# Performance work log

Hardware: AMD Instinct MI355X
Metric: run time of the kernel (lower is better)

The kernel has to match this reference:

```python
import jax, jax.numpy as jnp
import numpy as np

N, E, F_IN, HID, HEADS, OUT = 50000, 800000, 128, 64, 4, 40


def gat_layer(x, src, dst, n, W, a_src, a_dst, b, heads, ch):
    # PyG GATConv: h = x @ W per head; e_ij = LeakyReLU(a_src.h_j + a_dst.h_i)
    h = (x @ W).reshape(n, heads, ch)
    al_s = jnp.einsum('nhc,hc->nh', h, a_src)  # source-side logit term
    al_d = jnp.einsum('nhc,hc->nh', h, a_dst)  # target-side logit term
    e = jax.nn.leaky_relu(al_s[src] + al_d[dst], negative_slope=0.2)  # [E,H]
    m = jax.ops.segment_max(e, dst, num_segments=n)  # stable softmax per target node
    e = jnp.exp(e - m[dst])
    s = jax.ops.segment_sum(e, dst, num_segments=n)
    alpha = e / s[dst]  # [E,H]
    out = jax.ops.segment_sum(h[src] * alpha[:, :, None], dst, num_segments=n)  # [n,H,C]
    return out.reshape(n, heads * ch) + b


def gat_forward(x, src, dst, W0, as0, ad0, b0, W1, as1, ad1, b1, W2, as2, ad2, b2):
    n = x.shape[0]
    x = jax.nn.elu(gat_layer(x, src, dst, n, W0, as0, ad0, b0, HEADS, HID))
    x = jax.nn.elu(gat_layer(x, src, dst, n, W1, as1, ad1, b1, HEADS, HID))
    x = gat_layer(x, src, dst, n, W2, as2, ad2, b2, 1, OUT)
    return jax.nn.log_softmax(x, axis=1)


def setup_inputs() -> dict:
    key = jax.random.key(0)
    ks = jax.random.split(key, 16)
    x = jax.random.normal(ks[0], (N, F_IN), dtype=jnp.float32)
    edge_index = jax.random.randint(ks[1], (2, E), 0, N, dtype=jnp.int64)
    g = lambda k, sh: jax.random.normal(k, sh, dtype=jnp.float32) * (1.0 / np.sqrt(sh[0]))
    d_hid = HID * HEADS
    return {
        'x': x, 'edge_index': edge_index,
        'W0': g(ks[2], (F_IN, d_hid)), 'as0': g(ks[3], (HEADS, HID)), 'ad0': g(ks[4], (HEADS, HID)), 'b0': jnp.zeros((d_hid,), jnp.float32),
        'W1': g(ks[5], (d_hid, d_hid)), 'as1': g(ks[6], (HEADS, HID)), 'ad1': g(ks[7], (HEADS, HID)), 'b1': jnp.zeros((d_hid,), jnp.float32),
        'W2': g(ks[8], (d_hid, OUT)), 'as2': g(ks[9], (1, OUT)), 'ad2': g(ks[10], (1, OUT)), 'b2': jnp.zeros((OUT,), jnp.float32),
    }


def reference(x, edge_index, W0, as0, ad0, b0, W1, as1, ad1, b1, W2, as2, ad2, b2):
    n = x.shape[0]
    loops = jnp.arange(n, dtype=edge_index.dtype)  # PyG add_self_loops=True
    src = jnp.concatenate([edge_index[0], loops])
    dst = jnp.concatenate([edge_index[1], loops])
    return gat_forward(x, src, dst, W0, as0, ad0, b0, W1, as1, ad1, b1, W2, as2, ad2, b2)
```

## Files before the change

kernel.cpp:

```cpp
#include <hip/hip_runtime.h>
#include <hip/hip_fp16.h>
#include <math.h>

#define NODES 50000
#define NEDGES 800000
#define TOT_E (NEDGES + NODES)
#define SCAN_B 256
#define SCAN_NB ((NODES + SCAN_B - 1) / SCAN_B)

typedef __attribute__((ext_vector_type(8))) _Float16 half8v;
typedef __attribute__((ext_vector_type(4))) float f32x4;

union U2H { uint u; __half2 h; };

static __device__ __forceinline__ float lrelu(float z) {
  return z > 0.f ? z : 0.2f * z;
}
static __device__ __forceinline__ ushort f2h(float f) {
  __half h = __float2half_rn(f);
  return *reinterpret_cast<ushort*>(&h);
}
static __device__ __forceinline__ void wave_lds_fence() {
  __builtin_amdgcn_wave_barrier();
  asm volatile("s_waitcnt lgkmcnt(0)" ::: "memory");
  __builtin_amdgcn_sched_barrier(0);
}

static __device__ __forceinline__ void packB_one(const float* __restrict__ W,
    ushort* __restrict__ Bp, int N, int NF, int idx) {
  int i = idx & 7;
  int lane = (idx >> 3) & 63;
  int rem = idx >> 9;
  int nf = rem % NF;
  int kf = rem / NF;
  int k = kf * 32 + (lane >> 4) * 8 + i;
  int col = nf * 16 + (lane & 15);
  float v = (col < N) ? W[(size_t)k * N + col] : 0.f;
  Bp[idx] = f2h(v);
}

__global__ __launch_bounds__(256) void k_setup(const int* __restrict__ dst,
    int* __restrict__ counts, const float* __restrict__ x, ushort* __restrict__ xb0,
    const float* __restrict__ W0, ushort* __restrict__ Bp0,
    const float* __restrict__ W1, ushort* __restrict__ Bp1,
    const float* __restrict__ W2, ushort* __restrict__ Bp2) {
  int gb = blockIdx.x;
  int tid = threadIdx.x;
  if (gb < 2048) {
    int stride = 2048 * 256;
    for (int i = gb * 256 + tid; i < TOT_E; i += stride) {
      int d = (i < NEDGES) ? dst[i] : (i - NEDGES);
      atomicAdd(&counts[d], 1);
    }
  } else if (gb < 4048) {
    int total4 = NODES * 128 / 4;
    int stride = 2000 * 256;
    for (int i = (gb - 2048) * 256 + tid; i < total4; i += stride) {
      float4 v = *(const float4*)&x[i * 4];
      ushort4 o;
      o.x = f2h(v.x); o.y = f2h(v.y); o.z = f2h(v.z); o.w = f2h(v.w);
      *(ushort4*)&xb0[i * 4] = o;
    }
  } else {
    int b = gb - 4048;
    int stride = 48 * 256;
    int base = b * 256 + tid;
    for (int idx = base; idx < 4 * 16 * 512; idx += stride) packB_one(W0, Bp0, 256, 16, idx);
    for (int idx = base; idx < 8 * 16 * 512; idx += stride) packB_one(W1, Bp1, 256, 16, idx);
    for (int idx = base; idx < 8 * 3 * 512; idx += stride)  packB_one(W2, Bp2, 40, 3, idx);
  }
}

__global__ __launch_bounds__(SCAN_B) void k_scan_red(const int* __restrict__ counts,
                                                     int* __restrict__ bsum) {
  __shared__ int sm[SCAN_B];
  int idx = blockIdx.x * SCAN_B + threadIdx.x;
  int v = (idx < NODES) ? counts[idx] : 0;
  sm[threadIdx.x] = v;
  __syncthreads();
  for (int off = SCAN_B / 2; off > 0; off >>= 1) {
    if (threadIdx.x < off) sm[threadIdx.x] += sm[threadIdx.x + off];
    __syncthreads();
  }
  if (threadIdx.x == 0) bsum[blockIdx.x] = sm[0];
}

__global__ __launch_bounds__(256) void k_scan_part(const int* __restrict__ bsum,
                                                   int* __restrict__ bpre) {
  __shared__ int sm[256];
  int tid = threadIdx.x;
  int v = (tid < SCAN_NB) ? bsum[tid] : 0;
  sm[tid] = v;
  __syncthreads();
  for (int off = 1; off < 256; off <<= 1) {
    int t = (tid >= off) ? sm[tid - off] : 0;
    __syncthreads();
    sm[tid] += t;
    __syncthreads();
  }
  if (tid < SCAN_NB) bpre[tid] = sm[tid] - v;
}

__global__ __launch_bounds__(SCAN_B) void k_scan_emit(const int* __restrict__ counts,
    const int* __restrict__ bpre, int* __restrict__ offs, int* __restrict__ cur) {
  __shared__ int sm[SCAN_B];
  int idx = blockIdx.x * SCAN_B + threadIdx.x;
  int tid = threadIdx.x;
  int v = (idx < NODES) ? counts[idx] : 0;
  sm[tid] = v;
  __syncthreads();
  for (int off = 1; off < SCAN_B; off <<= 1) {
    int t = (tid >= off) ? sm[tid - off] : 0;
    __syncthreads();
    sm[tid] += t;
    __syncthreads();
  }
  int base = bpre[blockIdx.x];
  int excl = base + sm[tid] - v;
  if (idx < NODES) { offs[idx] = excl; cur[idx] = excl; }
  if (idx == NODES - 1) offs[NODES] = excl + v;
}

__global__ void k_scatter(const int* __restrict__ src, const int* __restrict__ dst,
                          int* __restrict__ cur, int* __restrict__ ssrc) {
  int stride = gridDim.x * blockDim.x;
  for (int i = blockIdx.x * blockDim.x + threadIdx.x; i < TOT_E; i += stride) {
    int s, d;
    if (i < NEDGES) { s = src[i]; d = dst[i]; } else { s = i - NEDGES; d = s; }
    int pos = atomicAdd(&cur[d], 1);
    ssrc[pos] = s;
  }
}

template<int KF, int NFW, int CG, int HEADS, int NF_TOT>
__global__ __launch_bounds__(256, 2) void k_gemm_reg(
    const ushort* __restrict__ A, const ushort* __restrict__ Bp,
    ushort* __restrict__ H, const float* __restrict__ a_s, const float* __restrict__ a_d,
    float* __restrict__ al_s, float* __restrict__ al_d, int M, int N, int K) {
  int wib = threadIdx.x >> 6;
  int lane = threadIdx.x & 63;
  int lg = lane >> 4;
  int lr = lane & 15;
  int cg, strip0, sstride;
  if (CG == 4) { cg = wib; strip0 = blockIdx.x; sstride = gridDim.x; }
  else { cg = 0; strip0 = blockIdx.x * 4 + wib; sstride = gridDim.x * 4; }

  half8v b[KF][NFW];
#pragma unroll
  for (int kf = 0; kf < KF; ++kf)
#pragma unroll
    for (int n = 0; n < NFW; ++n)
      b[kf][n] = *(const half8v*)(Bp + ((size_t)(kf * NF_TOT + cg * NFW + n) * 64 + lane) * 8);

  float asc[NFW], adc[NFW];
#pragma unroll
  for (int n = 0; n < NFW; ++n) {
    int col = (cg * NFW + n) * 16 + lr;
    bool ok = col < N;
    asc[n] = ok ? a_s[col] : 0.f;
    adc[n] = ok ? a_d[col] : 0.f;
  }

  int nstrips = M >> 4;
  for (int strip = strip0; strip < nstrips; strip += sstride) {
    const ushort* arow = A + (size_t)(strip * 16 + lr) * K + lg * 8;
    half8v a[KF];
#pragma unroll
    for (int kf = 0; kf < KF; ++kf) a[kf] = *(const half8v*)(arow + kf * 32);
    f32x4 acc[NFW];
#pragma unroll
    for (int n = 0; n < NFW; ++n) acc[n] = (f32x4){0.f, 0.f, 0.f, 0.f};
#pragma unroll
    for (int kf = 0; kf < KF; ++kf)
#pragma unroll
      for (int n = 0; n < NFW; ++n)
        acc[n] = __builtin_amdgcn_mfma_f32_16x16x32_f16(a[kf], b[kf][n], acc[n], 0, 0, 0);

#pragma unroll
    for (int n = 0; n < NFW; ++n) {
      int col = (cg * NFW + n) * 16 + lr;
      if (col < N) {
#pragma unroll
        for (int r = 0; r < 4; ++r) {
          int row = strip * 16 + lg * 4 + r;
          H[(size_t)row * N + col] = f2h(acc[n][r]);
        }
      }
    }

    float ps[4], pd[4];
#pragma unroll
    for (int r = 0; r < 4; ++r) {
      float s = 0.f, d = 0.f;
#pragma unroll
      for (int n = 0; n < NFW; ++n) {
        s += acc[n][r] * asc[n];
        d += acc[n][r] * adc[n];
      }
      ps[r] = s; pd[r] = d;
    }
#pragma unroll
    for (int off = 1; off <= 8; off <<= 1)
#pragma unroll
      for (int t = 0; t < 4; ++t) {
        ps[t] += __shfl_xor(ps[t], off);
        pd[t] += __shfl_xor(pd[t], off);
      }
    if (lr < 4) {
      int row = strip * 16 + lg * 4 + lr;
      if (HEADS == 4) {
        al_s[row * 4 + cg] = ps[lr];
        al_d[row * 4 + cg] = pd[lr];
      } else {
        al_s[row] = ps[lr];
        al_d[row] = pd[lr];
      }
    }
  }
}

__global__ __launch_bounds__(256) void k_agg4(const ushort* __restrict__ hb,
    const float* __restrict__ al_s, const float* __restrict__ al_d,
    const int* __restrict__ offs, const int* __restrict__ ssrc,
    const float* __restrict__ bias, ushort* __restrict__ outb) {
  __shared__ uint s_sv[8][32];
  __shared__ uint s_al[8][4][33];
  int hw = threadIdx.x >> 5;
  int node = (blockIdx.x * 256 + threadIdx.x) >> 5;
  if (node >= NODES) return;
  int l = threadIdx.x & 31;
  int beg = offs[node], end = offs[node + 1];
  float4 ald4 = *(const float4*)&al_d[node * 4];

  float m[4] = {-1e30f, -1e30f, -1e30f, -1e30f};
  for (int i = beg + l; i < end; i += 32) {
    int sv = ssrc[i];
    float4 a4 = *(const float4*)&al_s[sv * 4];
    m[0] = fmaxf(m[0], lrelu(a4.x + ald4.x));
    m[1] = fmaxf(m[1], lrelu(a4.y + ald4.y));
    m[2] = fmaxf(m[2], lrelu(a4.z + ald4.z));
    m[3] = fmaxf(m[3], lrelu(a4.w + ald4.w));
  }
#pragma unroll
  for (int off = 1; off <= 16; off <<= 1) {
#pragma unroll
    for (int h = 0; h < 4; ++h) m[h] = fmaxf(m[h], __shfl_xor(m[h], off));
  }

  int hh = l >> 3;
  uint clb = (uint)l * 8;
  float sacc[4] = {0.f, 0.f, 0.f, 0.f};
  __half2 z2 = __float2half2_rn(0.f);
  __half2 accA[4] = {z2, z2, z2, z2};
  __half2 accB[4] = {z2, z2, z2, z2};

  for (int cb = beg; cb < end; cb += 32) {
    int cnt = min(32, end - cb);
    wave_lds_fence();
    if (l < cnt) {
      uint sv = (uint)ssrc[cb + l];
      float4 a4 = *(const float4*)&al_s[sv * 4];
      float t0 = __expf(lrelu(a4.x + ald4.x) - m[0]);
      float t1 = __expf(lrelu(a4.y + ald4.y) - m[1]);
      float t2 = __expf(lrelu(a4.z + ald4.z) - m[2]);
      float t3 = __expf(lrelu(a4.w + ald4.w) - m[3]);
      sacc[0] += t0; sacc[1] += t1; sacc[2] += t2; sacc[3] += t3;
      U2H p0, p1, p2, p3;
      p0.h = __float2half2_rn(t0); p1.h = __float2half2_rn(t1);
      p2.h = __float2half2_rn(t2); p3.h = __float2half2_rn(t3);
      s_sv[hw][l] = sv;
      s_al[hw][0][l] = p0.u; s_al[hw][1][l] = p1.u;
      s_al[hw][2][l] = p2.u; s_al[hw][3][l] = p3.u;
    }
    wave_lds_fence();
    int e = 0;
    for (; e + 7 < cnt; e += 8) {
      uint sv0 = s_sv[hw][e],     sv1 = s_sv[hw][e + 1];
      uint sv2 = s_sv[hw][e + 2], sv3 = s_sv[hw][e + 3];
      uint sv4 = s_sv[hw][e + 4], sv5 = s_sv[hw][e + 5];
      uint sv6 = s_sv[hw][e + 6], sv7 = s_sv[hw][e + 7];
      U2H a0, a1, a2, a3, a4, a5, a6, a7;
      a0.u = s_al[hw][hh][e];     a1.u = s_al[hw][hh][e + 1];
      a2.u = s_al[hw][hh][e + 2]; a3.u = s_al[hw][hh][e + 3];
      a4.u = s_al[hw][hh][e + 4]; a5.u = s_al[hw][hh][e + 5];
      a6.u = s_al[hw][hh][e + 6]; a7.u = s_al[hw][hh][e + 7];
      uint4 hv0 = *(const uint4*)(hb + ((sv0 << 8) + clb));
      uint4 hv1 = *(const uint4*)(hb + ((sv1 << 8) + clb));
      uint4 hv2 = *(const uint4*)(hb + ((sv2 << 8) + clb));
      uint4 hv3 = *(const uint4*)(hb + ((sv3 << 8) + clb));
      uint4 hv4 = *(const uint4*)(hb + ((sv4 << 8) + clb));
      uint4 hv5 = *(const uint4*)(hb + ((sv5 << 8) + clb));
      uint4 hv6 = *(const uint4*)(hb + ((sv6 << 8) + clb));
      uint4 hv7 = *(const uint4*)(hb + ((sv7 << 8) + clb));
      U2H v;
      v.u = hv0.x; accA[0] = __hfma2(a0.h, v.h, accA[0]);
      v.u = hv0.y; accA[1] = __hfma2(a0.h, v.h, accA[1]);
      v.u = hv0.z; accA[2] = __hfma2(a0.h, v.h, accA[2]);
      v.u = hv0.w; accA[3] = __hfma2(a0.h, v.h, accA[3]);
      v.u = hv1.x; accB[0] = __hfma2(a1.h, v.h, accB[0]);
      v.u = hv1.y; accB[1] = __hfma2(a1.h, v.h, accB[1]);
      v.u = hv1.z; accB[2] = __hfma2(a1.h, v.h, accB[2]);
      v.u = hv1.w; accB[3] = __hfma2(a1.h, v.h, accB[3]);
      v.u = hv2.x; accA[0] = __hfma2(a2.h, v.h, accA[0]);
      v.u = hv2.y; accA[1] = __hfma2(a2.h, v.h, accA[1]);
      v.u = hv2.z; accA[2] = __hfma2(a2.h, v.h, accA[2]);
      v.u = hv2.w; accA[3] = __hfma2(a2.h, v.h, accA[3]);
      v.u = hv3.x; accB[0] = __hfma2(a3.h, v.h, accB[0]);
      v.u = hv3.y; accB[1] = __hfma2(a3.h, v.h, accB[1]);
      v.u = hv3.z; accB[2] = __hfma2(a3.h, v.h, accB[2]);
      v.u = hv3.w; accB[3] = __hfma2(a3.h, v.h, accB[3]);
      v.u = hv4.x; accA[0] = __hfma2(a4.h, v.h, accA[0]);
      v.u = hv4.y; accA[1] = __hfma2(a4.h, v.h, accA[1]);
      v.u = hv4.z; accA[2] = __hfma2(a4.h, v.h, accA[2]);
      v.u = hv4.w; accA[3] = __hfma2(a4.h, v.h, accA[3]);
      v.u = hv5.x; accB[0] = __hfma2(a5.h, v.h, accB[0]);
      v.u = hv5.y; accB[1] = __hfma2(a5.h, v.h, accB[1]);
      v.u = hv5.z; accB[2] = __hfma2(a5.h, v.h, accB[2]);
      v.u = hv5.w; accB[3] = __hfma2(a5.h, v.h, accB[3]);
      v.u = hv6.x; accA[0] = __hfma2(a6.h, v.h, accA[0]);
      v.u = hv6.y; accA[1] = __hfma2(a6.h, v.h, accA[1]);
      v.u = hv6.z; accA[2] = __hfma2(a6.h, v.h, accA[2]);
      v.u = hv6.w; accA[3] = __hfma2(a6.h, v.h, accA[3]);
      v.u = hv7.x; accB[0] = __hfma2(a7.h, v.h, accB[0]);
      v.u = hv7.y; accB[1] = __hfma2(a7.h, v.h, accB[1]);
      v.u = hv7.z; accB[2] = __hfma2(a7.h, v.h, accB[2]);
      v.u = hv7.w; accB[3] = __hfma2(a7.h, v.h, accB[3]);
    }
    for (; e + 3 < cnt; e += 4) {
      uint sv0 = s_sv[hw][e],     sv1 = s_sv[hw][e + 1];
      uint sv2 = s_sv[hw][e + 2], sv3 = s_sv[hw][e + 3];
      U2H a0, a1, a2, a3;
      a0.u = s_al[hw][hh][e];     a1.u = s_al[hw][hh][e + 1];
      a2.u = s_al[hw][hh][e + 2]; a3.u = s_al[hw][hh][e + 3];
      uint4 hv0 = *(const uint4*)(hb + ((sv0 << 8) + clb));
      uint4 hv1 = *(const uint4*)(hb + ((sv1 << 8) + clb));
      uint4 hv2 = *(const uint4*)(hb + ((sv2 << 8) + clb));
      uint4 hv3 = *(const uint4*)(hb + ((sv3 << 8) + clb));
      U2H v;
      v.u = hv0.x; accA[0] = __hfma2(a0.h, v.h, accA[0]);
      v.u = hv0.y; accA[1] = __hfma2(a0.h, v.h, accA[1]);
      v.u = hv0.z; accA[2] = __hfma2(a0.h, v.h, accA[2]);
      v.u = hv0.w; accA[3] = __hfma2(a0.h, v.h, accA[3]);
      v.u = hv1.x; accB[0] = __hfma2(a1.h, v.h, accB[0]);
      v.u = hv1.y; accB[1] = __hfma2(a1.h, v.h, accB[1]);
      v.u = hv1.z; accB[2] = __hfma2(a1.h, v.h, accB[2]);
      v.u = hv1.w; accB[3] = __hfma2(a1.h, v.h, accB[3]);
      v.u = hv2.x; accA[0] = __hfma2(a2.h, v.h, accA[0]);
      v.u = hv2.y; accA[1] = __hfma2(a2.h, v.h, accA[1]);
      v.u = hv2.z; accA[2] = __hfma2(a2.h, v.h, accA[2]);
      v.u = hv2.w; accA[3] = __hfma2(a2.h, v.h, accA[3]);
      v.u = hv3.x; accB[0] = __hfma2(a3.h, v.h, accB[0]);
      v.u = hv3.y; accB[1] = __hfma2(a3.h, v.h, accB[1]);
      v.u = hv3.z; accB[2] = __hfma2(a3.h, v.h, accB[2]);
      v.u = hv3.w; accB[3] = __hfma2(a3.h, v.h, accB[3]);
    }
    for (; e < cnt; ++e) {
      uint sv = s_sv[hw][e];
      U2H a0; a0.u = s_al[hw][hh][e];
      uint4 hv = *(const uint4*)(hb + ((sv << 8) + clb));
      U2H v;
      v.u = hv.x; accA[0] = __hfma2(a0.h, v.h, accA[0]);
      v.u = hv.y; accA[1] = __hfma2(a0.h, v.h, accA[1]);
      v.u = hv.z; accA[2] = __hfma2(a0.h, v.h, accA[2]);
      v.u = hv.w; accA[3] = __hfma2(a0.h, v.h, accA[3]);
    }
  }
#pragma unroll
  for (int off = 1; off <= 16; off <<= 1) {
#pragma unroll
    for (int h = 0; h < 4; ++h) sacc[h] += __shfl_xor(sacc[h], off);
  }
  float invs = 1.f / sacc[hh];
  ushort4 ores[2];
#pragma unroll
  for (int j = 0; j < 4; ++j) {
    U2H t; t.h = __hadd2(accA[j], accB[j]);
    float lo = __low2float(t.h) * invs + bias[l * 8 + j * 2];
    float hi = __high2float(t.h) * invs + bias[l * 8 + j * 2 + 1];
    lo = lo > 0.f ? lo : __expf(lo) - 1.f;
    hi = hi > 0.f ? hi : __expf(hi) - 1.f;
    ((ushort*)ores)[j * 2]     = f2h(lo);
    ((ushort*)ores)[j * 2 + 1] = f2h(hi);
  }
  *(ushort4*)(outb + (size_t)node * 256 + l * 8)     = ores[0];
  *(ushort4*)(outb + (size_t)node * 256 + l * 8 + 4) = ores[1];
}

__global__ __launch_bounds__(256) void k_agg1(const ushort* __restrict__ hb,
    const float* __restrict__ al_s, const float* __restrict__ al_d,
    const int* __restrict__ offs, const int* __restrict__ ssrc,
    const float* __restrict__ bias, float* __restrict__ out) {
  __shared__ uint s_sv[8][32];
  __shared__ uint s_al[8][32];
  int hw = threadIdx.x >> 5;
  int node = (blockIdx.x * 256 + threadIdx.x) >> 5;
  if (node >= NODES) return;
  int l = threadIdx.x & 31;
  int beg = offs[node], end = offs[node + 1];
  float ald = al_d[node];

  float m = -1e30f;
  for (int i = beg + l; i < end; i += 32)
    m = fmaxf(m, lrelu(al_s[ssrc[i]] + ald));
#pragma unroll
  for (int off = 1; off <= 16; off <<= 1) m = fmaxf(m, __shfl_xor(m, off));

  int p = l >> 4;
  int cq = l & 15;
  bool act = cq < 10;
  uint cqb = (uint)cq * 4;
  float sacc = 0.f;
  __half2 z2 = __float2half2_rn(0.f);
  __half2 accA[2] = {z2, z2};
  __half2 accB[2] = {z2, z2};
  for (int cb = beg; cb < end; cb += 32) {
    int cnt = min(32, end - cb);
    wave_lds_fence();
    if (l < cnt) {
      uint sv = (uint)ssrc[cb + l];
      float t = __expf(lrelu(al_s[sv] + ald) - m);
      sacc += t;
      U2H pk; pk.h = __float2half2_rn(t);
      s_sv[hw][l] = sv;
      s_al[hw][l] = pk.u;
    }
    wave_lds_fence();
    int e = p;
    for (; e + 6 < cnt; e += 8) {
      uint sv0 = s_sv[hw][e],     sv1 = s_sv[hw][e + 2];
      uint sv2 = s_sv[hw][e + 4], sv3 = s_sv[hw][e + 6];
      U2H a0, a1, a2, a3;
      a0.u = s_al[hw][e];     a1.u = s_al[hw][e + 2];
      a2.u = s_al[hw][e + 4]; a3.u = s_al[hw][e + 6];
      if (act) {
        uint2 hv0 = *(const uint2*)(hb + (sv0 * 40u + cqb));
        uint2 hv1 = *(const uint2*)(hb + (sv1 * 40u + cqb));
        uint2 hv2 = *(const uint2*)(hb + (sv2 * 40u + cqb));
        uint2 hv3 = *(const uint2*)(hb + (sv3 * 40u + cqb));
        U2H v;
        v.u = hv0.x; accA[0] = __hfma2(a0.h, v.h, accA[0]);
        v.u = hv0.y; accA[1] = __hfma2(a0.h, v.h, accA[1]);
        v.u = hv1.x; accB[0] = __hfma2(a1.h, v.h, accB[0]);
        v.u = hv1.y; accB[1] = __hfma2(a1.h, v.h, accB[1]);
        v.u = hv2.x; accA[0] = __hfma2(a2.h, v.h, accA[0]);
        v.u = hv2.y; accA[1] = __hfma2(a2.h, v.h, accA[1]);
        v.u = hv3.x; accB[0] = __hfma2(a3.h, v.h, accB[0]);
        v.u = hv3.y; accB[1] = __hfma2(a3.h, v.h, accB[1]);
      }
    }
    for (; e < cnt; e += 2) {
      uint sv = s_sv[hw][e];
      U2H a0; a0.u = s_al[hw][e];
      if (act) {
        uint2 hv = *(const uint2*)(hb + (sv * 40u + cqb));
        U2H v;
        v.u = hv.x; accA[0] = __hfma2(a0.h, v.h, accA[0]);
        v.u = hv.y; accA[1] = __hfma2(a0.h, v.h, accA[1]);
      }
    }
  }
#pragma unroll
  for (int off = 1; off <= 16; off <<= 1) sacc += __shfl_xor(sacc, off);
  float invs = 1.f / sacc;
  float vv[4];
#pragma unroll
  for (int j = 0; j < 2; ++j) {
    U2H t; t.h = __hadd2(accA[j], accB[j]);
    U2H o; o.u = __shfl_xor(t.u, 16);
    t.h = __hadd2(t.h, o.h);
    vv[j * 2]     = __low2float(t.h) * invs;
    vv[j * 2 + 1] = __high2float(t.h) * invs;
  }
  float mm = -1e30f;
  if (act) {
#pragma unroll
    for (int j = 0; j < 4; ++j) {
      vv[j] += bias[cq * 4 + j];
      mm = fmaxf(mm, vv[j]);
    }
  }
#pragma unroll
  for (int off = 1; off <= 8; off <<= 1) mm = fmaxf(mm, __shfl_xor(mm, off));
  float se = 0.f;
  if (act) {
#pragma unroll
    for (int j = 0; j < 4; ++j) se += __expf(vv[j] - mm);
  }
#pragma unroll
  for (int off = 1; off <= 8; off <<= 1) se += __shfl_xor(se, off);
  if (act && p == 0) {
    float lse = mm + __logf(se);
    float4 o;
    o.x = vv[0] - lse; o.y = vv[1] - lse; o.z = vv[2] - lse; o.w = vv[3] - lse;
    *(float4*)&out[(size_t)node * 40 + cq * 4] = o;
  }
}

extern "C" void kernel_launch(void* const* d_in, const int* in_sizes, int n_in,
                              void* d_out, int out_size, void* d_ws, size_t ws_size,
                              hipStream_t stream) {
  const float* x   = (const float*)d_in[0];
  const int*   ei  = (const int*)d_in[1];
  const float* W0  = (const float*)d_in[2];
  const float* as0 = (const float*)d_in[3];
  const float* ad0 = (const float*)d_in[4];
  const float* b0  = (const float*)d_in[5];
  const float* W1  = (const float*)d_in[6];
  const float* as1 = (const float*)d_in[7];
  const float* ad1 = (const float*)d_in[8];
  const float* b1  = (const float*)d_in[9];
  const float* W2  = (const float*)d_in[10];
  const float* as2 = (const float*)d_in[11];
  const float* ad2 = (const float*)d_in[12];
  const float* b2  = (const float*)d_in[13];
  float* out = (float*)d_out;

  char* p = (char*)d_ws;
  auto take = [&](size_t bytes) {
    char* q = p;
    p += (bytes + 255) & ~(size_t)255;
    return (void*)q;
  };
  ushort* xb0 = (ushort*)take((size_t)NODES * 128 * 2);
  ushort* xb1 = (ushort*)take((size_t)NODES * 256 * 2);
  ushort* xb2 = (ushort*)take((size_t)NODES * 256 * 2);
  ushort* hb  = (ushort*)take((size_t)NODES * 256 * 2);
  float* als  = (float*)take((size_t)NODES * 4 * 4);
  float* ald  = (float*)take((size_t)NODES * 4 * 4);
  int* ssrc   = (int*)take((size_t)TOT_E * 4);
  int* offs   = (int*)take((size_t)(NODES + 1) * 4);
  int* cur    = (int*)take((size_t)NODES * 4);
  int* cnt    = (int*)take((size_t)NODES * 4);
  int* bsum   = (int*)take((size_t)SCAN_NB * 4);
  int* bpre   = (int*)take((size_t)SCAN_NB * 4);
  ushort* Bp0 = (ushort*)take((size_t)4 * 16 * 512 * 2);
  ushort* Bp1 = (ushort*)take((size_t)8 * 16 * 512 * 2);
  ushort* Bp2 = (ushort*)take((size_t)8 * 3 * 512 * 2);

  hipMemsetAsync(cnt, 0, (size_t)NODES * 4, stream);
  k_setup<<<4096, 256, 0, stream>>>(ei + NEDGES, cnt, x, xb0, W0, Bp0, W1, Bp1, W2, Bp2);
  k_scan_red<<<SCAN_NB, SCAN_B, 0, stream>>>(cnt, bsum);
  k_scan_part<<<1, 256, 0, stream>>>(bsum, bpre);
  k_scan_emit<<<SCAN_NB, SCAN_B, 0, stream>>>(cnt, bpre, offs, cur);
  k_scatter<<<2048, 256, 0, stream>>>(ei, ei + NEDGES, cur, ssrc);

  int nab = (NODES * 32 + 255) / 256;

  k_gemm_reg<4, 4, 4, 4, 16><<<512, 256, 0, stream>>>(xb0, Bp0, hb, as0, ad0, als, ald, NODES, 256, 128);
  k_agg4<<<nab, 256, 0, stream>>>(hb, als, ald, offs, ssrc, b0, xb1);

  k_gemm_reg<8, 4, 4, 4, 16><<<512, 256, 0, stream>>>(xb1, Bp1, hb, as1, ad1, als, ald, NODES, 256, 256);
  k_agg4<<<nab, 256, 0, stream>>>(hb, als, ald, offs, ssrc, b1, xb2);

  k_gemm_reg<8, 3, 1, 1, 3><<<512, 256, 0, stream>>>(xb2, Bp2, hb, as2, ad2, als, ald, NODES, 40, 256);
  k_agg1<<<nab, 256, 0, stream>>>(hb, als, ald, offs, ssrc, b2, out);
}
```

Measured before the change: 306.6 us.

## Fuse scan phases, store CSR sources as ushort, unroll final aggregation

```diff
diff --git a/kernel.cpp b/kernel.cpp
--- a/kernel.cpp
+++ b/kernel.cpp
@@ -71,9 +71,10 @@
   }
 }
 
-__global__ __launch_bounds__(SCAN_B) void k_scan_red(const int* __restrict__ counts,
-                                                     int* __restrict__ bsum) {
+__global__ __launch_bounds__(SCAN_B) void k_scan_red_part(const int* __restrict__ counts,
+    int* __restrict__ bsum, int* __restrict__ bpre, int* __restrict__ done) {
   __shared__ int sm[SCAN_B];
+  __shared__ int lastflag;
   int idx = blockIdx.x * SCAN_B + threadIdx.x;
   int v = (idx < NODES) ? counts[idx] : 0;
   sm[threadIdx.x] = v;
@@ -82,23 +83,26 @@
     if (threadIdx.x < off) sm[threadIdx.x] += sm[threadIdx.x + off];
     __syncthreads();
   }
-  if (threadIdx.x == 0) bsum[blockIdx.x] = sm[0];
-}
-
-__global__ __launch_bounds__(256) void k_scan_part(const int* __restrict__ bsum,
-                                                   int* __restrict__ bpre) {
-  __shared__ int sm[256];
+  if (threadIdx.x == 0) {
+    __hip_atomic_store(&bsum[blockIdx.x], sm[0], __ATOMIC_RELEASE, __HIP_MEMORY_SCOPE_AGENT);
+    int t = __hip_atomic_fetch_add(done, 1, __ATOMIC_ACQ_REL, __HIP_MEMORY_SCOPE_AGENT);
+    lastflag = (t == (int)gridDim.x - 1);
+  }
+  __syncthreads();
+  if (!lastflag) return;
   int tid = threadIdx.x;
-  int v = (tid < SCAN_NB) ? bsum[tid] : 0;
-  sm[tid] = v;
+  int b = (tid < SCAN_NB)
+      ? __hip_atomic_load(&bsum[tid], __ATOMIC_ACQUIRE, __HIP_MEMORY_SCOPE_AGENT) : 0;
+  __syncthreads();
+  sm[tid] = b;
   __syncthreads();
   for (int off = 1; off < 256; off <<= 1) {
-    int t = (tid >= off) ? sm[tid - off] : 0;
+    int t2 = (tid >= off) ? sm[tid - off] : 0;
     __syncthreads();
-    sm[tid] += t;
+    sm[tid] += t2;
     __syncthreads();
   }
-  if (tid < SCAN_NB) bpre[tid] = sm[tid] - v;
+  if (tid < SCAN_NB) bpre[tid] = sm[tid] - b;
 }
 
 __global__ __launch_bounds__(SCAN_B) void k_scan_emit(const int* __restrict__ counts,
@@ -122,13 +126,13 @@
 }
 
 __global__ void k_scatter(const int* __restrict__ src, const int* __restrict__ dst,
-                          int* __restrict__ cur, int* __restrict__ ssrc) {
+                          int* __restrict__ cur, ushort* __restrict__ ssrc) {
   int stride = gridDim.x * blockDim.x;
   for (int i = blockIdx.x * blockDim.x + threadIdx.x; i < TOT_E; i += stride) {
     int s, d;
     if (i < NEDGES) { s = src[i]; d = dst[i]; } else { s = i - NEDGES; d = s; }
     int pos = atomicAdd(&cur[d], 1);
-    ssrc[pos] = s;
+    ssrc[pos] = (ushort)s;
   }
 }
 
@@ -221,7 +225,7 @@
 
 __global__ __launch_bounds__(256) void k_agg4(const ushort* __restrict__ hb,
     const float* __restrict__ al_s, const float* __restrict__ al_d,
-    const int* __restrict__ offs, const int* __restrict__ ssrc,
+    const int* __restrict__ offs, const ushort* __restrict__ ssrc,
     const float* __restrict__ bias, ushort* __restrict__ outb) {
   __shared__ uint s_sv[8][32];
   __shared__ uint s_al[8][4][33];
@@ -388,7 +392,7 @@
 
 __global__ __launch_bounds__(256) void k_agg1(const ushort* __restrict__ hb,
     const float* __restrict__ al_s, const float* __restrict__ al_d,
-    const int* __restrict__ offs, const int* __restrict__ ssrc,
+    const int* __restrict__ offs, const ushort* __restrict__ ssrc,
     const float* __restrict__ bias, float* __restrict__ out) {
   __shared__ uint s_sv[8][32];
   __shared__ uint s_al[8][32];
@@ -426,6 +430,44 @@
     }
     wave_lds_fence();
     int e = p;
+    for (; e + 14 < cnt; e += 16) {
+      uint sv0 = s_sv[hw][e],      sv1 = s_sv[hw][e + 2];
+      uint sv2 = s_sv[hw][e + 4],  sv3 = s_sv[hw][e + 6];
+      uint sv4 = s_sv[hw][e + 8],  sv5 = s_sv[hw][e + 10];
+      uint sv6 = s_sv[hw][e + 12], sv7 = s_sv[hw][e + 14];
+      U2H a0, a1, a2, a3, a4, a5, a6, a7;
+      a0.u = s_al[hw][e];      a1.u = s_al[hw][e + 2];
+      a2.u = s_al[hw][e + 4];  a3.u = s_al[hw][e + 6];
+      a4.u = s_al[hw][e + 8];  a5.u = s_al[hw][e + 10];
+      a6.u = s_al[hw][e + 12]; a7.u = s_al[hw][e + 14];
+      if (act) {
+        uint2 hv0 = *(const uint2*)(hb + (sv0 * 40u + cqb));
+        uint2 hv1 = *(const uint2*)(hb + (sv1 * 40u + cqb));
+        uint2 hv2 = *(const uint2*)(hb + (sv2 * 40u + cqb));
+        uint2 hv3 = *(const uint2*)(hb + (sv3 * 40u + cqb));
+        uint2 hv4 = *(const uint2*)(hb + (sv4 * 40u + cqb));
+        uint2 hv5 = *(const uint2*)(hb + (sv5 * 40u + cqb));
+        uint2 hv6 = *(const uint2*)(hb + (sv6 * 40u + cqb));
+        uint2 hv7 = *(const uint2*)(hb + (sv7 * 40u + cqb));
+        U2H v;
+        v.u = hv0.x; accA[0] = __hfma2(a0.h, v.h, accA[0]);
+        v.u = hv0.y; accA[1] = __hfma2(a0.h, v.h, accA[1]);
+        v.u = hv1.x; accB[0] = __hfma2(a1.h, v.h, accB[0]);
+        v.u = hv1.y; accB[1] = __hfma2(a1.h, v.h, accB[1]);
+        v.u = hv2.x; accA[0] = __hfma2(a2.h, v.h, accA[0]);
+        v.u = hv2.y; accA[1] = __hfma2(a2.h, v.h, accA[1]);
+        v.u = hv3.x; accB[0] = __hfma2(a3.h, v.h, accB[0]);
+        v.u = hv3.y; accB[1] = __hfma2(a3.h, v.h, accB[1]);
+        v.u = hv4.x; accA[0] = __hfma2(a4.h, v.h, accA[0]);
+        v.u = hv4.y; accA[1] = __hfma2(a4.h, v.h, accA[1]);
+        v.u = hv5.x; accB[0] = __hfma2(a5.h, v.h, accB[0]);
+        v.u = hv5.y; accB[1] = __hfma2(a5.h, v.h, accB[1]);
+        v.u = hv6.x; accA[0] = __hfma2(a6.h, v.h, accA[0]);
+        v.u = hv6.y; accA[1] = __hfma2(a6.h, v.h, accA[1]);
+        v.u = hv7.x; accB[0] = __hfma2(a7.h, v.h, accB[0]);
+        v.u = hv7.y; accB[1] = __hfma2(a7.h, v.h, accB[1]);
+      }
+    }
     for (; e + 6 < cnt; e += 8) {
       uint sv0 = s_sv[hw][e],     sv1 = s_sv[hw][e + 2];
       uint sv2 = s_sv[hw][e + 4], sv3 = s_sv[hw][e + 6];
@@ -527,22 +569,22 @@
   ushort* hb  = (ushort*)take((size_t)NODES * 256 * 2);
   float* als  = (float*)take((size_t)NODES * 4 * 4);
   float* ald  = (float*)take((size_t)NODES * 4 * 4);
-  int* ssrc   = (int*)take((size_t)TOT_E * 4);
+  ushort* ssrc= (ushort*)take((size_t)TOT_E * 2);
   int* offs   = (int*)take((size_t)(NODES + 1) * 4);
   int* cur    = (int*)take((size_t)NODES * 4);
-  int* cnt    = (int*)take((size_t)NODES * 4);
+  int* cnt    = (int*)take((size_t)(NODES + 64) * 4);
+  int* done   = cnt + NODES;
   int* bsum   = (int*)take((size_t)SCAN_NB * 4);
   int* bpre   = (int*)take((size_t)SCAN_NB * 4);
   ushort* Bp0 = (ushort*)take((size_t)4 * 16 * 512 * 2);
   ushort* Bp1 = (ushort*)take((size_t)8 * 16 * 512 * 2);
   ushort* Bp2 = (ushort*)take((size_t)8 * 3 * 512 * 2);
 
-  hipMemsetAsync(cnt, 0, (size_t)NODES * 4, stream);
+  hipMemsetAsync(cnt, 0, (size_t)(NODES + 64) * 4, stream);
   k_setup<<<4096, 256, 0, stream>>>(ei + NEDGES, cnt, x, xb0, W0, Bp0, W1, Bp1, W2, Bp2);
-  k_scan_red<<<SCAN_NB, SCAN_B, 0, stream>>>(cnt, bsum);
-  k_scan_part<<<1, 256, 0, stream>>>(bsum, bpre);
+  k_scan_red_part<<<SCAN_NB, SCAN_B, 0, stream>>>(cnt, bsum, bpre, done);
   k_scan_emit<<<SCAN_NB, SCAN_B, 0, stream>>>(cnt, bpre, offs, cur);
-  k_scatter<<<2048, 256, 0, stream>>>(ei, ei + NEDGES, cur, ssrc);
+  k_scatter<<<4096, 256, 0, stream>>>(ei, ei + NEDGES, cur, ssrc);
 
   int nab = (NODES * 32 + 255) / 256;
 
```

Measured after the change: 296.2 us. 3.4% less time.
